# Kernel tuning notes

Hardware: AMD Instinct MI355X
Metric: run time of the kernel (lower is better)

The kernel has to match this reference:

```python
import jax, jax.numpy as jnp
import numpy as np
import math

B, S, D, H, DFF = 4, 2048, 1024, 16, 4096
DK = D // H
EPS = 1e-5

def setup_inputs() -> dict:
    key = jax.random.key(0)
    ks = jax.random.split(key, 16)
    s_d = 1.0 / math.sqrt(D)
    s_ff = 1.0 / math.sqrt(DFF)
    return {
        "x": jax.random.normal(ks[0], (B, S, D), jnp.float32),
        "wq": jax.random.uniform(ks[1], (D, D), jnp.float32, -s_d, s_d),
        "bq": jnp.zeros((D,), jnp.float32),
        "wk": jax.random.uniform(ks[2], (D, D), jnp.float32, -s_d, s_d),
        "bk": jnp.zeros((D,), jnp.float32),
        "wv": jax.random.uniform(ks[3], (D, D), jnp.float32, -s_d, s_d),
        "bv": jnp.zeros((D,), jnp.float32),
        "wo": jax.random.uniform(ks[4], (D, D), jnp.float32, -s_d, s_d),
        "bo": jnp.zeros((D,), jnp.float32),
        "w1": jax.random.uniform(ks[5], (DFF, D), jnp.float32, -s_d, s_d),
        "b1": jnp.zeros((DFF,), jnp.float32),
        "w2": jax.random.uniform(ks[6], (D, DFF), jnp.float32, -s_ff, s_ff),
        "b2": jnp.zeros((D,), jnp.float32),
        "ln1_g": jnp.ones((D,), jnp.float32),
        "ln1_b": jnp.zeros((D,), jnp.float32),
        "ln2_g": jnp.ones((D,), jnp.float32),
        "ln2_b": jnp.zeros((D,), jnp.float32),
    }

def _layernorm(x, g, b):
    mu = jnp.mean(x, axis=-1, keepdims=True)
    var = jnp.mean(jnp.square(x - mu), axis=-1, keepdims=True)
    return (x - mu) * jax.lax.rsqrt(var + EPS) * g + b

def reference(x, wq, bq, wk, bk, wv, bv, wo, bo, w1, b1, w2, b2, ln1_g, ln1_b, ln2_g, ln2_b):
    # Multi-head self-attention (dropout in eval mode -> identity).
    Q = (x @ wq.T + bq).reshape(B, S, H, DK).transpose(0, 2, 1, 3)  # (B,H,S,DK)
    K = (x @ wk.T + bk).reshape(B, S, H, DK).transpose(0, 2, 1, 3)
    V = (x @ wv.T + bv).reshape(B, S, H, DK).transpose(0, 2, 1, 3)
    scores = jnp.einsum('bhqd,bhkd->bhqk', Q, K) / math.sqrt(DK)  # (B,H,S,S)
    attn = jax.nn.softmax(scores, axis=-1)
    ctx = jnp.einsum('bhqk,bhkd->bhqd', attn, V)
    ctx = ctx.transpose(0, 2, 1, 3).reshape(B, S, D)
    attn_out = ctx @ wo.T + bo
    # SkipConnection: x + norm(sublayer)  (post-applied LayerNorm on sublayer output)
    x = x + _layernorm(attn_out, ln1_g, ln1_b)
    # FFN
    ff = jax.nn.relu(x @ w1.T + b1) @ w2.T + b2
    return x + _layernorm(ff, ln2_g, ln2_b)
```

## Files before the change

### kernel.cpp

```cpp
#include <hip/hip_runtime.h>
#include <hip/hip_bf16.h>
#include <stdint.h>


#define DI __device__ __forceinline__

typedef __attribute__((ext_vector_type(4))) float f32x4;
typedef __attribute__((ext_vector_type(16))) float f32x16;
typedef __attribute__((ext_vector_type(8))) short bf16x8;
typedef __attribute__((ext_vector_type(4))) short s16x4;

#define B_ 4
#define S_ 2048
#define D_ 1024
#define H_ 16
#define DK_ 64
#define DFF_ 4096
#define M_ 8192

DI float bf2f(short s) {
  union { unsigned u; float f; } v;
  v.u = ((unsigned)(unsigned short)s) << 16;
  return v.f;
}
DI short f2bf(float f) {
  union { float f; unsigned u; } v;
  v.f = f;
  unsigned r = v.u + 0x7FFFu + ((v.u >> 16) & 1u);
  return (short)(r >> 16);
}
DI unsigned pkbf(float lo, float hi) {
  unsigned r;
  asm("v_cvt_pk_bf16_f32 %0, %1, %2" : "=v"(r) : "v"(lo), "v"(hi));
  return r;
}
DI void plswap(unsigned& a, unsigned& b) {
  asm volatile("v_permlane32_swap_b32 %0, %1" : "+v"(a), "+v"(b));
}

__global__ __launch_bounds__(256) void cvt_kernel(const float* __restrict__ in,
                                                  short* __restrict__ out, int n) {
  long i = ((long)blockIdx.x * blockDim.x + threadIdx.x) * 8;
  if (i >= n) return;
  f32x4 a = *(const f32x4*)(in + i);
  f32x4 b = *(const f32x4*)(in + i + 4);
  bf16x8 r;
  r[0] = f2bf(a[0]); r[1] = f2bf(a[1]); r[2] = f2bf(a[2]); r[3] = f2bf(a[3]);
  r[4] = f2bf(b[0]); r[5] = f2bf(b[1]); r[6] = f2bf(b[2]); r[7] = f2bf(b[3]);
  *(bf16x8*)(out + i) = r;
}

DI void gl_lds16(const void* g, void* l) {
  __builtin_amdgcn_global_load_lds(
      (const __attribute__((address_space(1))) unsigned int*)g,
      (__attribute__((address_space(3))) unsigned int*)l, 16, 0, 0);
}

template <int MODE>
__global__ __launch_bounds__(256, 2)
void gemm_bt(const short* __restrict__ A, const short* __restrict__ Bm,
             const float* __restrict__ bias0, const float* __restrict__ bias1,
             const float* __restrict__ bias2, short* __restrict__ C,
             int M, int N, int K,
             short* __restrict__ Qo, short* __restrict__ Ko, short* __restrict__ Vo) {
  __shared__ short As[128 * 32];
  __shared__ short Bs[128 * 32];
  const int t = threadIdx.x, w = t >> 6, l = t & 63;
  const int row0 = blockIdx.y * 128, col0 = blockIdx.x * 128;
  const int wr = (w >> 1) * 64, wc = (w & 1) * 64;
  const int lr = l & 15, lk = l >> 4;

  f32x4 acc[4][4] = {};

  const int e0 = (w * 64 + l) * 8;
  const int e1 = ((4 + w) * 64 + l) * 8;
  const int ar0 = e0 >> 5, ac0 = e0 & 31;
  const int ar1 = e1 >> 5, ac1 = e1 & 31;
  short* la0 = &As[w * 512];
  short* la1 = &As[(4 + w) * 512];
  short* lb0 = &Bs[w * 512];
  short* lb1 = &Bs[(4 + w) * 512];
  const short* Ab = A + (long)row0 * K;
  const short* Bb = Bm + (long)col0 * K;

  for (int k0 = 0; k0 < K; k0 += 32) {
    __syncthreads();
    gl_lds16(Ab + (long)ar0 * K + k0 + ac0, la0);
    gl_lds16(Ab + (long)ar1 * K + k0 + ac1, la1);
    gl_lds16(Bb + (long)ar0 * K + k0 + ac0, lb0);
    gl_lds16(Bb + (long)ar1 * K + k0 + ac1, lb1);
    __syncthreads();
    bf16x8 af[4], bfr[4];
#pragma unroll
    for (int m = 0; m < 4; ++m)
      af[m] = *(const bf16x8*)&As[(wr + m * 16 + lr) * 32 + lk * 8];
#pragma unroll
    for (int n = 0; n < 4; ++n)
      bfr[n] = *(const bf16x8*)&Bs[(wc + n * 16 + lr) * 32 + lk * 8];
#pragma unroll
    for (int m = 0; m < 4; ++m)
#pragma unroll
      for (int n = 0; n < 4; ++n)
        acc[m][n] =
            __builtin_amdgcn_mfma_f32_16x16x32_bf16(af[m], bfr[n], acc[m][n], 0, 0, 0);
  }

  if (MODE == 2) {
    const int which = col0 >> 10;
#pragma unroll
    for (int m = 0; m < 4; ++m) {
#pragma unroll
      for (int n = 0; n < 4; ++n) {
        const int r0 = row0 + wr + m * 16 + lk * 4;
        const int c = col0 + wc + n * 16 + lr;
        const int cc = c & 1023;
        const int h = cc >> 6, dk = cc & 63;
        const int bb = r0 >> 11, s = r0 & 2047;
        if (which == 2) {
          const float bias = bias2[cc];
          s16x4 v4;
#pragma unroll
          for (int j = 0; j < 4; ++j) v4[j] = f2bf(acc[m][n][j] + bias);
          *(s16x4*)(Vo + ((long)((bb * H_ + h) * DK_ + dk)) * S_ + s) = v4;
        } else {
          const float bias = (which == 0 ? bias0[cc] : bias1[cc]);
          const float sc = (which == 0 ? 0.125f : 1.0f);
          short* dst = (which == 0 ? Qo : Ko);
#pragma unroll
          for (int j = 0; j < 4; ++j)
            dst[(((long)(bb * H_ + h) * S_) + s + j) * DK_ + dk] =
                f2bf((acc[m][n][j] + bias) * sc);
        }
      }
    }
  } else {
#pragma unroll
    for (int m = 0; m < 4; ++m) {
#pragma unroll
      for (int n = 0; n < 4; ++n) {
#pragma unroll
        for (int j = 0; j < 4; ++j) {
          int r = row0 + wr + m * 16 + lk * 4 + j;
          int c = col0 + wc + n * 16 + lr;
          float v = acc[m][n][j] + bias0[c];
          if (MODE == 1) v = fmaxf(v, 0.0f);
          C[(long)r * N + c] = f2bf(v);
        }
      }
    }
  }
}

__global__ __launch_bounds__(256, 3)
void attn_kernel(const short* __restrict__ Q, const short* __restrict__ K,
                 const short* __restrict__ Vt, short* __restrict__ ctx) {
  __shared__ short Ks[64 * 64];
  __shared__ short Vs[64 * 64];
  const int t = threadIdx.x, w = t >> 6, l = t & 63;
  const int q31 = l & 31, hi = l >> 5;
  const int bh = blockIdx.y;
  const int q0 = blockIdx.x * 128 + w * 32;
  const long base = (long)bh * S_ * DK_;

  bf16x8 qf[4];
  {
    const short* qp = Q + base + (long)(q0 + q31) * DK_ + hi * 8;
#pragma unroll
    for (int ks = 0; ks < 4; ++ks) qf[ks] = *(const bf16x8*)(qp + ks * 16);
  }

  f32x16 oa[2] = {};
  float mrun = -1e30f, lrun = 0.0f;

  const int srow = l >> 3;
  const int scol = ((l & 7) ^ srow) * 8;
  short* ldsK0 = &Ks[w * 1024];
  short* ldsK1 = &Ks[w * 1024 + 512];
  short* ldsV0 = &Vs[w * 1024];
  short* ldsV1 = &Vs[w * 1024 + 512];
  const int kr0 = w * 16 + srow, kr1 = w * 16 + 8 + srow;

  for (int kv0 = 0; kv0 < S_; kv0 += 64) {
    __syncthreads();
    gl_lds16(K + base + (long)(kv0 + kr0) * DK_ + scol, ldsK0);
    gl_lds16(K + base + (long)(kv0 + kr1) * DK_ + scol, ldsK1);
    gl_lds16(Vt + base + (long)kr0 * S_ + kv0 + scol, ldsV0);
    gl_lds16(Vt + base + (long)kr1 * S_ + kv0 + scol, ldsV1);
    __syncthreads();

    f32x16 sacc[2] = {};
#pragma unroll
    for (int m = 0; m < 2; ++m) {
      const int row = m * 32 + q31;
      const int sw = row & 7;
#pragma unroll
      for (int ks = 0; ks < 4; ++ks) {
        bf16x8 kf = *(const bf16x8*)&Ks[row * 64 + (((2 * ks + hi) ^ sw) << 3)];
        sacc[m] = __builtin_amdgcn_mfma_f32_32x32x16_bf16(kf, qf[ks], sacc[m], 0, 0, 0);
      }
    }

    float tm = sacc[0][0];
#pragma unroll
    for (int r = 1; r < 16; ++r) tm = fmaxf(tm, sacc[0][r]);
#pragma unroll
    for (int r = 0; r < 16; ++r) tm = fmaxf(tm, sacc[1][r]);
    tm = fmaxf(tm, __shfl_xor(tm, 32, 64));
    const float mnew = fmaxf(mrun, tm);
    const float fac = __expf(mrun - mnew);
    float ps = 0.0f;
#pragma unroll
    for (int m = 0; m < 2; ++m)
#pragma unroll
      for (int r = 0; r < 16; ++r) {
        float p = __expf(sacc[m][r] - mnew);
        sacc[m][r] = p;
        ps += p;
      }
    ps += __shfl_xor(ps, 32, 64);
    lrun = lrun * fac + ps;
    mrun = mnew;
#pragma unroll
    for (int m = 0; m < 2; ++m)
#pragma unroll
      for (int r = 0; r < 16; ++r) oa[m][r] *= fac;

    bf16x8 pf[4];
#pragma unroll
    for (int m = 0; m < 2; ++m)
#pragma unroll
      for (int sb = 0; sb < 2; ++sb) {
        unsigned p0 = pkbf(sacc[m][8 * sb + 0], sacc[m][8 * sb + 1]);
        unsigned p1 = pkbf(sacc[m][8 * sb + 2], sacc[m][8 * sb + 3]);
        unsigned p2 = pkbf(sacc[m][8 * sb + 4], sacc[m][8 * sb + 5]);
        unsigned p3 = pkbf(sacc[m][8 * sb + 6], sacc[m][8 * sb + 7]);
        plswap(p0, p2);
        plswap(p1, p3);
        union { unsigned u[4]; bf16x8 v; } fb;
        fb.u[0] = p0; fb.u[1] = p1; fb.u[2] = p2; fb.u[3] = p3;
        pf[2 * m + sb] = fb.v;
      }

#pragma unroll
    for (int mt = 0; mt < 2; ++mt) {
      const int row = mt * 32 + q31;
      const int sw = row & 7;
#pragma unroll
      for (int s = 0; s < 4; ++s) {
        bf16x8 vf = *(const bf16x8*)&Vs[row * 64 + (((2 * s + hi) ^ sw) << 3)];
        oa[mt] = __builtin_amdgcn_mfma_f32_32x32x16_bf16(vf, pf[s], oa[mt], 0, 0, 0);
      }
    }
  }

  const int bb2 = bh >> 4, h = bh & 15;
  const float rl = 1.0f / lrun;
  short* crow = ctx + ((long)(bb2 * S_ + q0 + q31)) * D_ + h * 64 + 4 * hi;
#pragma unroll
  for (int mt = 0; mt < 2; ++mt)
#pragma unroll
    for (int g = 0; g < 4; ++g) {
      s16x4 v4;
#pragma unroll
      for (int i = 0; i < 4; ++i) v4[i] = f2bf(oa[mt][4 * g + i] * rl);
      *(s16x4*)(crow + mt * 32 + g * 8) = v4;
    }
}

template <int RES_BF16, int OUT_BF16>
__global__ __launch_bounds__(256)
void add_ln(const void* __restrict__ resv, const short* __restrict__ a,
            const float* __restrict__ gam, const float* __restrict__ bet,
            void* __restrict__ outv) {
  const int row = blockIdx.x, t = threadIdx.x;
  const int w = t >> 6, l = t & 63;
  const long roff = (long)row * D_;
  const int c = t * 4;
  s16x4 av = *(const s16x4*)(a + roff + c);
  float v0 = bf2f(av[0]), v1 = bf2f(av[1]), v2 = bf2f(av[2]), v3 = bf2f(av[3]);
  float s = v0 + v1 + v2 + v3;
#pragma unroll
  for (int mask = 1; mask < 64; mask <<= 1) s += __shfl_xor(s, mask, 64);
  __shared__ float r1[4], r2[4];
  if (l == 0) r1[w] = s;
  __syncthreads();
  float mu = (r1[0] + r1[1] + r1[2] + r1[3]) * (1.0f / D_);
  float d0 = v0 - mu, d1 = v1 - mu, d2 = v2 - mu, d3 = v3 - mu;
  float sq = d0 * d0 + d1 * d1 + d2 * d2 + d3 * d3;
#pragma unroll
  for (int mask = 1; mask < 64; mask <<= 1) sq += __shfl_xor(sq, mask, 64);
  if (l == 0) r2[w] = sq;
  __syncthreads();
  float var = (r2[0] + r2[1] + r2[2] + r2[3]) * (1.0f / D_);
  float rs = rsqrtf(var + 1e-5f);
  float res0, res1, res2, res3;
  if (RES_BF16) {
    s16x4 rv = *(const s16x4*)((const short*)resv + roff + c);
    res0 = bf2f(rv[0]); res1 = bf2f(rv[1]); res2 = bf2f(rv[2]); res3 = bf2f(rv[3]);
  } else {
    f32x4 rv = *(const f32x4*)((const float*)resv + roff + c);
    res0 = rv[0]; res1 = rv[1]; res2 = rv[2]; res3 = rv[3];
  }
  float o0 = res0 + d0 * rs * gam[c + 0] + bet[c + 0];
  float o1 = res1 + d1 * rs * gam[c + 1] + bet[c + 1];
  float o2 = res2 + d2 * rs * gam[c + 2] + bet[c + 2];
  float o3 = res3 + d3 * rs * gam[c + 3] + bet[c + 3];
  if (OUT_BF16) {
    s16x4 ov;
    ov[0] = f2bf(o0); ov[1] = f2bf(o1); ov[2] = f2bf(o2); ov[3] = f2bf(o3);
    *(s16x4*)((short*)outv + roff + c) = ov;
  } else {
    f32x4 ov;
    ov[0] = o0; ov[1] = o1; ov[2] = o2; ov[3] = o3;
    *(f32x4*)((float*)outv + roff + c) = ov;
  }
}

extern "C" void kernel_launch(void* const* d_in, const int* in_sizes, int n_in,
                              void* d_out, int out_size, void* d_ws, size_t ws_size,
                              hipStream_t stream) {
  (void)in_sizes; (void)n_in; (void)out_size; (void)ws_size;
  const float* x   = (const float*)d_in[0];
  const float* wq  = (const float*)d_in[1];
  const float* bq  = (const float*)d_in[2];
  const float* wk  = (const float*)d_in[3];
  const float* bk  = (const float*)d_in[4];
  const float* wv  = (const float*)d_in[5];
  const float* bv  = (const float*)d_in[6];
  const float* wo  = (const float*)d_in[7];
  const float* bo  = (const float*)d_in[8];
  const float* w1  = (const float*)d_in[9];
  const float* b1  = (const float*)d_in[10];
  const float* w2  = (const float*)d_in[11];
  const float* b2  = (const float*)d_in[12];
  const float* g1  = (const float*)d_in[13];
  const float* be1 = (const float*)d_in[14];
  const float* g2  = (const float*)d_in[15];
  const float* be2 = (const float*)d_in[16];

  char* ws = (char*)d_ws;
  const long MB = 1 << 20;
  short* xb    = (short*)(ws + 0 * MB);
  short* wqkvb = (short*)(ws + 16 * MB);
  short* wob   = (short*)(ws + 22 * MB);
  short* w1b   = (short*)(ws + 24 * MB);
  short* w2b   = (short*)(ws + 32 * MB);
  short* Qb    = (short*)(ws + 40 * MB);
  short* Kb    = (short*)(ws + 56 * MB);
  short* Vtb   = (short*)(ws + 72 * MB);
  short* ctxb  = (short*)(ws + 88 * MB);
  short* aout  = (short*)(ws + 40 * MB);
  short* x1b   = (short*)(ws + 56 * MB);
  short* hid   = (short*)(ws + 88 * MB);
  short* ffb   = (short*)(ws + 72 * MB);

  auto cvt = [&](const float* in, short* out, long n) {
    cvt_kernel<<<dim3((unsigned)((n / 8 + 255) / 256)), dim3(256), 0, stream>>>(in, out, (int)n);
  };
  cvt(x, xb, (long)M_ * D_);
  cvt(wq, wqkvb + 0L * D_ * D_, (long)D_ * D_);
  cvt(wk, wqkvb + 1L * D_ * D_, (long)D_ * D_);
  cvt(wv, wqkvb + 2L * D_ * D_, (long)D_ * D_);
  cvt(wo, wob, (long)D_ * D_);
  cvt(w1, w1b, (long)DFF_ * D_);
  cvt(w2, w2b, (long)D_ * DFF_);

  gemm_bt<2><<<dim3(3072 / 128, M_ / 128), 256, 0, stream>>>(
      xb, wqkvb, bq, bk, bv, nullptr, M_, 3072, D_, Qb, Kb, Vtb);

  attn_kernel<<<dim3(S_ / 128, B_ * H_), 256, 0, stream>>>(Qb, Kb, Vtb, ctxb);

  gemm_bt<0><<<dim3(D_ / 128, M_ / 128), 256, 0, stream>>>(
      ctxb, wob, bo, nullptr, nullptr, aout, M_, D_, D_, nullptr, nullptr, nullptr);

  add_ln<0, 1><<<dim3(M_), 256, 0, stream>>>(x, aout, g1, be1, x1b);

  gemm_bt<1><<<dim3(DFF_ / 128, M_ / 128), 256, 0, stream>>>(
      x1b, w1b, b1, nullptr, nullptr, hid, M_, DFF_, D_, nullptr, nullptr, nullptr);
  gemm_bt<0><<<dim3(D_ / 128, M_ / 128), 256, 0, stream>>>(
      hid, w2b, b2, nullptr, nullptr, ffb, M_, D_, DFF_, nullptr, nullptr, nullptr);

  add_ln<1, 0><<<dim3(M_), 256, 0, stream>>>(x1b, ffb, g2, be2, d_out);
}
```

Before: 432.3 us.

## Replace GEMM with 8-wave double-buffered 256-row tiles, LDS swizzle, and XCD remap

Replaces the simple 128x128 single-buffered GEMM with an 8-wave kernel using 256xBN tiles and K-step 64. Global-to-LDS loads are double buffered with explicit vmcnt waits so the next stage's loads overlap the MFMA work. LDS rows are XOR-swizzled to avoid bank conflicts. Block indices are remapped so neighbouring tiles land on the same XCD for L2 reuse. The larger tiles give more data reuse, but they raise register and LDS pressure and produce fewer blocks for the N=1024 GEMMs.

After: 451.3 us. 4.4% more time.

```diff
diff --git a/kernel.cpp b/kernel.cpp
--- a/kernel.cpp
+++ b/kernel.cpp
@@ -56,63 +56,130 @@
       (__attribute__((address_space(3))) unsigned int*)l, 16, 0, 0);
 }
 
-template <int MODE>
-__global__ __launch_bounds__(256, 2)
-void gemm_bt(const short* __restrict__ A, const short* __restrict__ Bm,
-             const float* __restrict__ bias0, const float* __restrict__ bias1,
-             const float* __restrict__ bias2, short* __restrict__ C,
-             int M, int N, int K,
-             short* __restrict__ Qo, short* __restrict__ Ko, short* __restrict__ Vo) {
-  __shared__ short As[128 * 32];
-  __shared__ short Bs[128 * 32];
+
+#define RD_A(MH)                                                              \
+  _Pragma("unroll") for (int m = 0; m < 4; ++m) {                             \
+    const int lrow = (MH)*64 + m*16 + lr;                                     \
+    const int sw = lrow & 7;                                                  \
+    afr[m][0] = *(const bf16x8*)(aw + lrow*64 + ((lk ^ sw) << 3));            \
+    afr[m][1] = *(const bf16x8*)(aw + lrow*64 + (((4 + lk) ^ sw) << 3));      \
+  }
+
+#define RD_B(NBASE)                                                           \
+  _Pragma("unroll") for (int n = 0; n < NHF; ++n) {                           \
+    const int lrow = (wn & 1)*WN + ((NBASE) + n)*16 + lr;                     \
+    const int sw = lrow & 7;                                                  \
+    bfr[n][0] = *(const bf16x8*)(bw + lrow*64 + ((lk ^ sw) << 3));            \
+    bfr[n][1] = *(const bf16x8*)(bw + lrow*64 + (((4 + lk) ^ sw) << 3));      \
+  }
+
+#define MMA(MH, NBASE)                                                        \
+  __builtin_amdgcn_s_barrier();                                               \
+  asm volatile("s_waitcnt lgkmcnt(0)" ::: "memory");                          \
+  __builtin_amdgcn_sched_barrier(0);                                          \
+  __builtin_amdgcn_s_setprio(1);                                              \
+  _Pragma("unroll") for (int m = 0; m < 4; ++m)                               \
+    _Pragma("unroll") for (int n = 0; n < NHF; ++n) {                         \
+      acc[(MH)*4 + m][(NBASE) + n] = __builtin_amdgcn_mfma_f32_16x16x32_bf16( \
+          afr[m][0], bfr[n][0], acc[(MH)*4 + m][(NBASE) + n], 0, 0, 0);       \
+      acc[(MH)*4 + m][(NBASE) + n] = __builtin_amdgcn_mfma_f32_16x16x32_bf16( \
+          afr[m][1], bfr[n][1], acc[(MH)*4 + m][(NBASE) + n], 0, 0, 0);       \
+    }                                                                         \
+  __builtin_amdgcn_s_setprio(0);                                              \
+  __builtin_amdgcn_s_barrier();
+
+template <int BN, int MODE>
+__global__ __launch_bounds__(512, 2)
+void gemm8p(const short* __restrict__ A, const short* __restrict__ Bm,
+            const float* __restrict__ bias0, const float* __restrict__ bias1,
+            const float* __restrict__ bias2, short* __restrict__ C,
+            int M, int N, int K,
+            short* __restrict__ Qo, short* __restrict__ Ko, short* __restrict__ Vo) {
+  constexpr int NF = BN / 64;
+  constexpr int NHF = NF / 2;
+  constexpr int WN = BN / 4;
+  constexpr int BHALF = BN / 2;
+  constexpr int BLD = BN / 128;
+
+  __shared__ short As[2 * 256 * 64];
+  __shared__ short Bs[2 * BN * 64];
+
   const int t = threadIdx.x, w = t >> 6, l = t & 63;
-  const int row0 = blockIdx.y * 128, col0 = blockIdx.x * 128;
-  const int wr = (w >> 1) * 64, wc = (w & 1) * 64;
+  const int wm = w >> 2, wn = w & 3;
   const int lr = l & 15, lk = l >> 4;
 
-  f32x4 acc[4][4] = {};
-
-  const int e0 = (w * 64 + l) * 8;
-  const int e1 = ((4 + w) * 64 + l) * 8;
-  const int ar0 = e0 >> 5, ac0 = e0 & 31;
-  const int ar1 = e1 >> 5, ac1 = e1 & 31;
-  short* la0 = &As[w * 512];
-  short* la1 = &As[(4 + w) * 512];
-  short* lb0 = &Bs[w * 512];
-  short* lb1 = &Bs[(4 + w) * 512];
-  const short* Ab = A + (long)row0 * K;
-  const short* Bb = Bm + (long)col0 * K;
-
-  for (int k0 = 0; k0 < K; k0 += 32) {
-    __syncthreads();
-    gl_lds16(Ab + (long)ar0 * K + k0 + ac0, la0);
-    gl_lds16(Ab + (long)ar1 * K + k0 + ac1, la1);
-    gl_lds16(Bb + (long)ar0 * K + k0 + ac0, lb0);
-    gl_lds16(Bb + (long)ar1 * K + k0 + ac1, lb1);
-    __syncthreads();
-    bf16x8 af[4], bfr[4];
-#pragma unroll
-    for (int m = 0; m < 4; ++m)
-      af[m] = *(const bf16x8*)&As[(wr + m * 16 + lr) * 32 + lk * 8];
-#pragma unroll
-    for (int n = 0; n < 4; ++n)
-      bfr[n] = *(const bf16x8*)&Bs[(wc + n * 16 + lr) * 32 + lk * 8];
-#pragma unroll
-    for (int m = 0; m < 4; ++m)
-#pragma unroll
-      for (int n = 0; n < 4; ++n)
-        acc[m][n] =
-            __builtin_amdgcn_mfma_f32_16x16x32_bf16(af[m], bfr[n], acc[m][n], 0, 0, 0);
+  const int gx = gridDim.x;
+  const int nwg = gx * gridDim.y;
+  const int orig = blockIdx.y * gx + blockIdx.x;
+  const int lin = (orig & 7) * (nwg >> 3) + (orig >> 3);
+  const int row0 = (lin / gx) * 256;
+  const int col0 = (lin % gx) * BN;
+
+  const int NT = K >> 6;
+
+  const int c0 = w * 64 + l;
+  const int gr0 = c0 >> 3, gs0 = ((c0 & 7) ^ (gr0 & 7)) << 3;
+  const int c1 = 512 + c0;
+  const int gr1 = c1 >> 3, gs1 = ((c1 & 7) ^ (gr1 & 7)) << 3;
+  const short* A00 = A + (long)(row0 + gr0) * K + gs0;
+  const short* A01 = A + (long)(row0 + gr1) * K + gs1;
+  const short* A10 = A + (long)(row0 + 128 + gr0) * K + gs0;
+  const short* A11 = A + (long)(row0 + 128 + gr1) * K + gs1;
+  const short* Bsrc00 = Bm + (long)(col0 + gr0) * K + gs0;
+  const short* Bsrc01 = Bm + (long)(col0 + gr1) * K + gs1;
+  const short* Bsrc10 = Bm + (long)(col0 + BHALF + gr0) * K + gs0;
+  const short* Bsrc11 = Bm + (long)(col0 + BHALF + gr1) * K + gs1;
+
+  const int ldw0 = (w * 64) * 8;
+  const int ldw1 = (512 + w * 64) * 8;
+
+  auto stage = [&](int kt) {
+    const int koff = kt << 6;
+    short* Ab = As + (kt & 1) * 16384;
+    short* Bb = Bs + (kt & 1) * (BN * 64);
+    gl_lds16(A00 + koff, Ab + ldw0);
+    gl_lds16(A01 + koff, Ab + ldw1);
+    gl_lds16(A10 + koff, Ab + 8192 + ldw0);
+    gl_lds16(A11 + koff, Ab + 8192 + ldw1);
+    gl_lds16(Bsrc00 + koff, Bb + ldw0);
+    if (BLD == 2) gl_lds16(Bsrc01 + koff, Bb + ldw1);
+    gl_lds16(Bsrc10 + koff, Bb + BHALF * 64 + ldw0);
+    if (BLD == 2) gl_lds16(Bsrc11 + koff, Bb + BHALF * 64 + ldw1);
+  };
+
+  f32x4 acc[8][NF] = {};
+  bf16x8 afr[4][2], bfr[NHF][2];
+  const short* aw;
+  const short* bw;
+
+  stage(0);
+  stage(1);
+
+  for (int kt = 0; kt < NT; ++kt) {
+    if (kt + 1 < NT) {
+      if constexpr (BN == 256) asm volatile("s_waitcnt vmcnt(8)" ::: "memory");
+      else                     asm volatile("s_waitcnt vmcnt(6)" ::: "memory");
+    } else {
+      asm volatile("s_waitcnt vmcnt(0)" ::: "memory");
+    }
+    __builtin_amdgcn_s_barrier();
+    aw = As + (kt & 1) * 16384 + wm * 8192;
+    bw = Bs + (kt & 1) * (BN * 64) + (wn >> 1) * (BHALF * 64);
+    RD_A(0) RD_B(0) MMA(0, 0)
+    RD_B(NHF)       MMA(0, NHF)
+    RD_A(1)         MMA(1, NHF)
+    RD_B(0)         MMA(1, 0)
+    if (kt + 2 < NT) stage(kt + 2);
   }
 
   if (MODE == 2) {
     const int which = col0 >> 10;
 #pragma unroll
-    for (int m = 0; m < 4; ++m) {
-#pragma unroll
-      for (int n = 0; n < 4; ++n) {
-        const int r0 = row0 + wr + m * 16 + lk * 4;
-        const int c = col0 + wc + n * 16 + lr;
+    for (int m = 0; m < 8; ++m) {
+#pragma unroll
+      for (int n = 0; n < NF; ++n) {
+        const int r0 = row0 + wm * 128 + m * 16 + lk * 4;
+        const int c = col0 + wn * WN + n * 16 + lr;
         const int cc = c & 1023;
         const int h = cc >> 6, dk = cc & 63;
         const int bb = r0 >> 11, s = r0 & 2047;
@@ -135,13 +202,13 @@
     }
   } else {
 #pragma unroll
-    for (int m = 0; m < 4; ++m) {
-#pragma unroll
-      for (int n = 0; n < 4; ++n) {
+    for (int m = 0; m < 8; ++m) {
+#pragma unroll
+      for (int n = 0; n < NF; ++n) {
 #pragma unroll
         for (int j = 0; j < 4; ++j) {
-          int r = row0 + wr + m * 16 + lk * 4 + j;
-          int c = col0 + wc + n * 16 + lr;
+          const int r = row0 + wm * 128 + m * 16 + lk * 4 + j;
+          const int c = col0 + wn * WN + n * 16 + lr;
           float v = acc[m][n][j] + bias0[c];
           if (MODE == 1) v = fmaxf(v, 0.0f);
           C[(long)r * N + c] = f2bf(v);
@@ -365,19 +432,19 @@
   cvt(w1, w1b, (long)DFF_ * D_);
   cvt(w2, w2b, (long)D_ * DFF_);
 
-  gemm_bt<2><<<dim3(3072 / 128, M_ / 128), 256, 0, stream>>>(
+  gemm8p<256, 2><<<dim3(3072 / 256, M_ / 256), 512, 0, stream>>>(
       xb, wqkvb, bq, bk, bv, nullptr, M_, 3072, D_, Qb, Kb, Vtb);
 
   attn_kernel<<<dim3(S_ / 128, B_ * H_), 256, 0, stream>>>(Qb, Kb, Vtb, ctxb);
 
-  gemm_bt<0><<<dim3(D_ / 128, M_ / 128), 256, 0, stream>>>(
+  gemm8p<128, 0><<<dim3(D_ / 128, M_ / 256), 512, 0, stream>>>(
       ctxb, wob, bo, nullptr, nullptr, aout, M_, D_, D_, nullptr, nullptr, nullptr);
 
   add_ln<0, 1><<<dim3(M_), 256, 0, stream>>>(x, aout, g1, be1, x1b);
 
-  gemm_bt<1><<<dim3(DFF_ / 128, M_ / 128), 256, 0, stream>>>(
+  gemm8p<256, 1><<<dim3(DFF_ / 256, M_ / 256), 512, 0, stream>>>(
       x1b, w1b, b1, nullptr, nullptr, hid, M_, DFF_, D_, nullptr, nullptr, nullptr);
-  gemm_bt<0><<<dim3(D_ / 128, M_ / 128), 256, 0, stream>>>(
+  gemm8p<128, 0><<<dim3(D_ / 128, M_ / 256), 512, 0, stream>>>(
       hid, w2b, b2, nullptr, nullptr, ffb, M_, D_, DFF_, nullptr, nullptr, nullptr);
 
   add_ln<1, 0><<<dim3(M_), 256, 0, stream>>>(x1b, ffb, g2, be2, d_out);
```
